# Optimization experiments

Measured on AMD Instinct MI355X. Metric: run time of the kernel, lower is better.

Reference implementation:

```python
import jax, jax.numpy as jnp
import numpy as np

LAMB_MAX = 2.0


def cheb_conv_k2(x, edge_index, w0, w1, b):
    """PyG ChebConv with K=2, sym normalization, given lambda_max.
    out = x @ w0 + (L_hat x) @ w1 + b, where
    L_hat = (2/lmax) * (I - D^{-1/2} A D^{-1/2}) - I.
    """
    n = x.shape[0]
    src, dst = edge_index[0], edge_index[1]
    ew = jnp.ones(src.shape, x.dtype)
    deg = jax.ops.segment_sum(ew, src, num_segments=n)
    dinv = jnp.where(deg > 0, jax.lax.rsqrt(jnp.maximum(deg, 1e-12)), 0.0)
    s = 2.0 / LAMB_MAX
    # off-diagonal weights of scaled Laplacian: -s * d_i^{-1/2} d_j^{-1/2}
    norm = (-s) * dinv[src] * dinv[dst]  # [E]
    # gather-scale-scatter: (L_hat x)_offdiag
    agg = jax.ops.segment_sum(norm[:, None] * x[src], dst, num_segments=n)  # [N, F]
    tx1 = (s - 1.0) * x + agg  # diagonal: s*1 (L diag) + (-1) self-loop
    return x @ w0 + tx1 @ w1 + b


def setup_inputs() -> dict:
    key = jax.random.key(0)
    ks = jax.random.split(key, 8)
    N, E, F, H = 100000, 1600000, 128, 128
    x = jax.random.normal(ks[0], (N, F), dtype=jnp.float32)
    edge_index = jax.random.randint(ks[1], (2, E), 0, N, dtype=jnp.int32)
    # glorot-ish init for the two Chebyshev linear weights per layer
    sc1 = (2.0 / (F + H)) ** 0.5
    sc2 = (2.0 / (H + 1)) ** 0.5
    w1_0 = jax.random.normal(ks[2], (F, H), dtype=jnp.float32) * sc1
    w1_1 = jax.random.normal(ks[3], (F, H), dtype=jnp.float32) * sc1
    b1 = jnp.zeros((H,), jnp.float32)
    w2_0 = jax.random.normal(ks[4], (H, 1), dtype=jnp.float32) * sc2
    w2_1 = jax.random.normal(ks[5], (H, 1), dtype=jnp.float32) * sc2
    b2 = jnp.zeros((1,), jnp.float32)
    return {"x": x, "edge_index": edge_index, "w1_0": w1_0, "w1_1": w1_1,
            "b1": b1, "w2_0": w2_0, "w2_1": w2_1, "b2": b2}


def reference(x, edge_index, w1_0, w1_1, b1, w2_0, w2_1, b2):
    h = jax.nn.relu(cheb_conv_k2(x, edge_index, w1_0, w1_1, b1))
    out = jax.nn.sigmoid(cheb_conv_k2(h, edge_index, w2_0, w2_1, b2))
    return out  # [N, 1]
```

## Files before the change

### kernel.cpp

```cpp
#include <hip/hip_runtime.h>
#include <math.h>

#define F 128
#define SCAN_CHUNK 1024
#define CHUNK 32
#define NBLK 128

typedef __attribute__((ext_vector_type(8))) short bf16x8;
typedef __attribute__((ext_vector_type(4))) float f32x4;

__device__ inline unsigned short f2bf(float v) {
  unsigned u = __float_as_uint(v);
  unsigned r = (u + 0x7FFFu + ((u >> 16) & 1u)) >> 16;
  return (unsigned short)r;
}
__device__ inline float bf2f(unsigned short s) {
  return __uint_as_float(((unsigned)s) << 16);
}

__global__ __launch_bounds__(1024) void k_prep2(const int* __restrict__ src,
                                                const int* __restrict__ dst,
                                                const float* __restrict__ x,
                                                unsigned short* __restrict__ xb,
                                                int* __restrict__ cntgD,
                                                int* __restrict__ cntgS, int E,
                                                int NF4, int nb, int per) {
  extern __shared__ int smem[];
  int* cd = smem;
  int* cs = smem + nb;
  int blk = blockIdx.x;
  int tid = threadIdx.x;
  for (int b = tid; b < nb; b += 1024) {
    cd[b] = 0;
    cs[b] = 0;
  }
  __syncthreads();
  int e0 = blk * per;
  int e1 = e0 + per;
  if (e1 > E) e1 = E;
  for (int e = e0 + tid; e < e1; e += 1024) {
    atomicAdd(&cd[dst[e] >> 7], 1);
    atomicAdd(&cs[src[e] >> 7], 1);
  }
  const float4* x4 = (const float4*)x;
  ushort4* xb4 = (ushort4*)xb;
  for (int i = blk * 1024 + tid; i < NF4; i += NBLK * 1024) {
    float4 v = x4[i];
    ushort4 o;
    o.x = f2bf(v.x);
    o.y = f2bf(v.y);
    o.z = f2bf(v.z);
    o.w = f2bf(v.w);
    xb4[i] = o;
  }
  __syncthreads();
  for (int b = tid; b < nb; b += 1024) {
    cntgD[b * NBLK + blk] = cd[b];
    cntgS[b * NBLK + blk] = cs[b];
  }
}

__global__ __launch_bounds__(NBLK) void k_scanBk2(int* __restrict__ cntgD,
                                                  int* __restrict__ cntgS,
                                                  int* __restrict__ totD,
                                                  int* __restrict__ totS, int nb) {
  __shared__ int sh[NBLK];
  int b = blockIdx.x;
  int tid = threadIdx.x;
  int* cntg;
  int* tot;
  int bb;
  if (b < nb) {
    cntg = cntgD;
    tot = totD;
    bb = b;
  } else {
    cntg = cntgS;
    tot = totS;
    bb = b - nb;
  }
  int v = cntg[bb * NBLK + tid];
  int val = v;
  sh[tid] = val;
  __syncthreads();
  for (int off = 1; off < NBLK; off <<= 1) {
    int o = (tid >= off) ? sh[tid - off] : 0;
    __syncthreads();
    val += o;
    sh[tid] = val;
    __syncthreads();
  }
  cntg[bb * NBLK + tid] = val - v;
  if (tid == NBLK - 1) tot[bb] = val;
}

__global__ __launch_bounds__(1024) void k_scanTot(const int* __restrict__ totD,
                                                  const int* __restrict__ totS,
                                                  int* __restrict__ baseD,
                                                  int* __restrict__ baseS, int nb,
                                                  int E) {
  __shared__ int sh[1024];
  int tid = threadIdx.x;
  int v = (tid < nb) ? totD[tid] : 0;
  int val = v;
  sh[tid] = val;
  __syncthreads();
  for (int off = 1; off < 1024; off <<= 1) {
    int o = (tid >= off) ? sh[tid - off] : 0;
    __syncthreads();
    val += o;
    sh[tid] = val;
    __syncthreads();
  }
  if (tid < nb) baseD[tid] = val - v;
  if (tid == 0) baseD[nb] = E;
  __syncthreads();
  v = (tid < nb) ? totS[tid] : 0;
  val = v;
  sh[tid] = val;
  __syncthreads();
  for (int off = 1; off < 1024; off <<= 1) {
    int o = (tid >= off) ? sh[tid - off] : 0;
    __syncthreads();
    val += o;
    sh[tid] = val;
    __syncthreads();
  }
  if (tid < nb) baseS[tid] = val - v;
  if (tid == 0) baseS[nb] = E;
}

__global__ __launch_bounds__(1024) void k_binfill2(
    const int* __restrict__ src, const int* __restrict__ dst,
    const int* __restrict__ cntgD, const int* __restrict__ cntgS,
    const int* __restrict__ baseD, const int* __restrict__ baseS,
    unsigned* __restrict__ binnedD, unsigned char* __restrict__ binnedS, int E,
    int nb, int per) {
  extern __shared__ int smem[];
  int* bD = smem;
  int* cD = smem + nb;
  int* bS = smem + 2 * nb;
  int* cS = smem + 3 * nb;
  int blk = blockIdx.x;
  for (int b = threadIdx.x; b < nb; b += 1024) {
    bD[b] = baseD[b] + cntgD[b * NBLK + blk];
    cD[b] = 0;
    bS[b] = baseS[b] + cntgS[b * NBLK + blk];
    cS[b] = 0;
  }
  __syncthreads();
  int e0 = blk * per;
  int e1 = e0 + per;
  if (e1 > E) e1 = E;
  for (int e = e0 + threadIdx.x; e < e1; e += 1024) {
    int s = src[e];
    int d = dst[e];
    int bk = d >> 7;
    int rk = atomicAdd(&cD[bk], 1);
    binnedD[bD[bk] + rk] = ((unsigned)s << 7) | (unsigned)(d & 127);
    int bs = s >> 7;
    int rs = atomicAdd(&cS[bs], 1);
    binnedS[bS[bs] + rs] = (unsigned char)(s & 127);
  }
}

__global__ __launch_bounds__(256) void k_csr(const unsigned char* __restrict__ binnedS,
                                             const int* __restrict__ baseS,
                                             const unsigned* __restrict__ binnedD,
                                             const int* __restrict__ baseD,
                                             float* __restrict__ dinv,
                                             int* __restrict__ rp,
                                             int* __restrict__ pairs, int N, int E) {
  __shared__ int cnt[128];
  __shared__ int sc[256];
  __shared__ int cur[128];
  int b = blockIdx.x;
  int tid = threadIdx.x;
  int node0 = b << 7;
  if (tid < 128) cnt[tid] = 0;
  __syncthreads();
  int sbeg = baseS[b], send = baseS[b + 1];
  for (int j = sbeg + tid; j < send; j += 256) atomicAdd(&cnt[binnedS[j]], 1);
  __syncthreads();
  if (tid < 128) {
    int node = node0 + tid;
    if (node < N) {
      int c = cnt[tid];
      dinv[node] = c > 0 ? rsqrtf((float)c) : 0.0f;
    }
    cnt[tid] = 0;
  }
  __syncthreads();
  int wbeg = baseD[b], wend = baseD[b + 1];
  for (int j = wbeg + tid; j < wend; j += 256) atomicAdd(&cnt[binnedD[j] & 127u], 1);
  __syncthreads();
  int v = (tid < 128) ? cnt[tid] : 0;
  int val = v;
  sc[tid] = val;
  __syncthreads();
  for (int off = 1; off < 128; off <<= 1) {
    int o = (tid >= off) ? sc[tid - off] : 0;
    __syncthreads();
    val += o;
    sc[tid] = val;
    __syncthreads();
  }
  if (tid < 128) {
    int excl = wbeg + val - v;
    int node = node0 + tid;
    if (node < N) rp[node] = excl;
    cur[tid] = excl;
  }
  if (b == 0 && tid == 0) rp[N] = E;
  __syncthreads();
  for (int j = wbeg + tid; j < wend; j += 256) {
    unsigned e = binnedD[j];
    int idx = atomicAdd(&cur[e & 127u], 1);
    pairs[idx] = (int)(e >> 7);
  }
}

__global__ __launch_bounds__(256) void k_prep(const int* __restrict__ src,
                                              const int* __restrict__ dst,
                                              const float* __restrict__ x,
                                              int* __restrict__ degA,
                                              int* __restrict__ degB,
                                              unsigned short* __restrict__ xb,
                                              int E, int NF4) {
  int t0 = blockIdx.x * 256 + threadIdx.x;
  int stride = gridDim.x * 256;
  for (int i = t0; i < E; i += stride) {
    atomicAdd(&degA[src[i]], 1);
    atomicAdd(&degB[dst[i]], 1);
  }
  const float4* x4 = (const float4*)x;
  ushort4* xb4 = (ushort4*)xb;
  for (int i = t0; i < NF4; i += stride) {
    float4 v = x4[i];
    ushort4 o;
    o.x = f2bf(v.x);
    o.y = f2bf(v.y);
    o.z = f2bf(v.z);
    o.w = f2bf(v.w);
    xb4[i] = o;
  }
}

__global__ __launch_bounds__(256) void k_scanA(const int* __restrict__ deg,
                                               int* __restrict__ rp,
                                               int* __restrict__ bsum, int N) {
  __shared__ int sh[256];
  int tid = threadIdx.x;
  int base = blockIdx.x * SCAN_CHUNK + tid * 4;
  int v0 = 0, v1 = 0, v2 = 0, v3 = 0;
  if (base + 0 < N) v0 = deg[base + 0];
  if (base + 1 < N) v1 = deg[base + 1];
  if (base + 2 < N) v2 = deg[base + 2];
  if (base + 3 < N) v3 = deg[base + 3];
  int ts = v0 + v1 + v2 + v3;
  int val = ts;
  sh[tid] = val;
  __syncthreads();
  for (int off = 1; off < 256; off <<= 1) {
    int other = (tid >= off) ? sh[tid - off] : 0;
    __syncthreads();
    val += other;
    sh[tid] = val;
    __syncthreads();
  }
  int excl = val - ts;
  if (base + 0 < N) rp[base + 0] = excl;
  if (base + 1 < N) rp[base + 1] = excl + v0;
  if (base + 2 < N) rp[base + 2] = excl + v0 + v1;
  if (base + 3 < N) rp[base + 3] = excl + v0 + v1 + v2;
  if (tid == 255) bsum[blockIdx.x] = val;
}

__global__ __launch_bounds__(256) void k_scanB(int* __restrict__ bsum, int nb) {
  __shared__ int sh[256];
  int tid = threadIdx.x;
  int ts = (tid < nb) ? bsum[tid] : 0;
  int val = ts;
  sh[tid] = val;
  __syncthreads();
  for (int off = 1; off < 256; off <<= 1) {
    int other = (tid >= off) ? sh[tid - off] : 0;
    __syncthreads();
    val += other;
    sh[tid] = val;
    __syncthreads();
  }
  if (tid < nb) bsum[tid] = val - ts;
}

__global__ __launch_bounds__(256) void k_scanC(int* __restrict__ rp,
                                               const int* __restrict__ bsum,
                                               int* __restrict__ pos,
                                               const int* __restrict__ degA,
                                               float* __restrict__ dinv, int N,
                                               int E) {
  int i = blockIdx.x * 256 + threadIdx.x;
  if (i < N) {
    int v = rp[i] + bsum[i >> 10];
    rp[i] = v;
    pos[i] = v;
    int d = degA[i];
    dinv[i] = d > 0 ? rsqrtf((float)d) : 0.0f;
  }
  if (i == 0) rp[N] = E;
}

__global__ __launch_bounds__(256) void k_fill(const int* __restrict__ src,
                                              const int* __restrict__ dst,
                                              int* __restrict__ pos,
                                              int* __restrict__ pairs, int E) {
  for (int e = blockIdx.x * 256 + threadIdx.x; e < E; e += gridDim.x * 256) {
    int s = src[e];
    int d = dst[e];
    int idx = atomicAdd(&pos[d], 1);
    pairs[idx] = s;
  }
}

__global__ __launch_bounds__(256) void k_gather1c(
    const int* __restrict__ pairs, const int* __restrict__ rp,
    const unsigned short* __restrict__ xb, const float* __restrict__ dinv,
    unsigned short* __restrict__ tb, int N) {
  int node = (blockIdx.x * 256 + threadIdx.x) >> 5;
  if (node >= N) return;
  int li = threadIdx.x & 31;
  int beg = rp[node], end = rp[node + 1];
  const uint2* x2 = (const uint2*)xb;
  float a0 = 0.f, a1 = 0.f, a2 = 0.f, a3 = 0.f;
  int j = beg;
  for (; j + 3 < end; j += 4) {
    int s0 = pairs[j], s1 = pairs[j + 1], s2 = pairs[j + 2], s3 = pairs[j + 3];
    float w0 = dinv[s0], w1 = dinv[s1], w2 = dinv[s2], w3 = dinv[s3];
    uint2 v0 = x2[(size_t)s0 * 32 + li];
    uint2 v1 = x2[(size_t)s1 * 32 + li];
    uint2 v2 = x2[(size_t)s2 * 32 + li];
    uint2 v3 = x2[(size_t)s3 * 32 + li];
    a0 += w0 * bf2f((unsigned short)v0.x) + w1 * bf2f((unsigned short)v1.x) +
          w2 * bf2f((unsigned short)v2.x) + w3 * bf2f((unsigned short)v3.x);
    a1 += w0 * bf2f((unsigned short)(v0.x >> 16)) +
          w1 * bf2f((unsigned short)(v1.x >> 16)) +
          w2 * bf2f((unsigned short)(v2.x >> 16)) +
          w3 * bf2f((unsigned short)(v3.x >> 16));
    a2 += w0 * bf2f((unsigned short)v0.y) + w1 * bf2f((unsigned short)v1.y) +
          w2 * bf2f((unsigned short)v2.y) + w3 * bf2f((unsigned short)v3.y);
    a3 += w0 * bf2f((unsigned short)(v0.y >> 16)) +
          w1 * bf2f((unsigned short)(v1.y >> 16)) +
          w2 * bf2f((unsigned short)(v2.y >> 16)) +
          w3 * bf2f((unsigned short)(v3.y >> 16));
  }
  for (; j < end; ++j) {
    int s0 = pairs[j];
    float w0 = dinv[s0];
    uint2 v0 = x2[(size_t)s0 * 32 + li];
    a0 += w0 * bf2f((unsigned short)v0.x);
    a1 += w0 * bf2f((unsigned short)(v0.x >> 16));
    a2 += w0 * bf2f((unsigned short)v0.y);
    a3 += w0 * bf2f((unsigned short)(v0.y >> 16));
  }
  float nd = -dinv[node];
  uint2 o;
  o.x = ((unsigned)f2bf(nd * a1) << 16) | f2bf(nd * a0);
  o.y = ((unsigned)f2bf(nd * a3) << 16) | f2bf(nd * a2);
  ((uint2*)tb)[(size_t)node * 32 + li] = o;
}

__global__ __launch_bounds__(256) void k_layer_mfma(
    const unsigned short* __restrict__ xb, const unsigned short* __restrict__ tb,
    const float* __restrict__ dinv, const float* __restrict__ w10,
    const float* __restrict__ w11, const float* __restrict__ b1,
    const float* __restrict__ w20, const float* __restrict__ w21,
    float* __restrict__ p, float* __restrict__ r, int N) {
  __shared__ __align__(16) short Ax[8 * 16 * 40];
  __shared__ __align__(16) short At[8 * 16 * 40];
  __shared__ float p_sh[CHUNK], r_sh[CHUNK];

  const int tid = threadIdx.x;
  const int wave = tid >> 6;
  const int lane = tid & 63;
  const int quad = lane >> 4;
  const int col = lane & 15;

  bf16x8 B0[4][2], B1[4][2];
  float b1f[2], w20f[2], w21f[2];
#pragma unroll
  for (int nt = 0; nt < 2; ++nt) {
    int f = wave * 32 + nt * 16 + col;
    b1f[nt] = b1[f];
    w20f[nt] = w20[f];
    w21f[nt] = w21[f];
  }
#pragma unroll
  for (int ks = 0; ks < 4; ++ks) {
#pragma unroll
    for (int nt = 0; nt < 2; ++nt) {
      int f = wave * 32 + nt * 16 + col;
      bf16x8 h0, h1;
#pragma unroll
      for (int j = 0; j < 8; ++j) {
        h0[j] = (short)f2bf(w10[(ks * 32 + quad * 8 + j) * F + f]);
        h1[j] = (short)f2bf(w11[(ks * 32 + quad * 8 + j) * F + f]);
      }
      B0[ks][nt] = h0;
      B1[ks][nt] = h1;
    }
  }

  const int nchunks = (N + CHUNK - 1) / CHUNK;
  for (int chunk = blockIdx.x; chunk < nchunks; chunk += gridDim.x) {
    int node0 = chunk * CHUNK;
    __syncthreads();

    {
      int nloc = tid >> 3;
      int k0 = (tid & 7) * 16;
      int gn = node0 + nloc;
      int mt = nloc >> 4, m = nloc & 15, ks = k0 >> 5, koff = k0 & 31;
      int base = ((mt * 4 + ks) * 16 + m) * 40 + koff;
      const uint2* xr = (const uint2*)(xb + (size_t)gn * F + k0);
      const uint2* tr = (const uint2*)(tb + (size_t)gn * F + k0);
      bool ok = (gn < N);
#pragma unroll
      for (int q4 = 0; q4 < 4; ++q4) {
        uint2 xv = ok ? xr[q4] : make_uint2(0u, 0u);
        uint2 tv = ok ? tr[q4] : make_uint2(0u, 0u);
        *(uint2*)&Ax[base + q4 * 4] = xv;
        *(uint2*)&At[base + q4 * 4] = tv;
      }
      if (tid < CHUNK) {
        p_sh[tid] = 0.f;
        r_sh[tid] = 0.f;
      }
    }
    __syncthreads();

    f32x4 acc[2][2];
#pragma unroll
    for (int mt = 0; mt < 2; ++mt)
#pragma unroll
      for (int nt = 0; nt < 2; ++nt) acc[mt][nt] = (f32x4)0.f;

#pragma unroll
    for (int mt = 0; mt < 2; ++mt) {
#pragma unroll
      for (int ks = 0; ks < 4; ++ks) {
        int ab = ((mt * 4 + ks) * 16 + col) * 40 + quad * 8;
        bf16x8 ax = *(bf16x8*)&Ax[ab];
        bf16x8 at = *(bf16x8*)&At[ab];
#pragma unroll
        for (int nt = 0; nt < 2; ++nt) {
          f32x4 c = acc[mt][nt];
          c = __builtin_amdgcn_mfma_f32_16x16x32_bf16(ax, B0[ks][nt], c, 0, 0, 0);
          c = __builtin_amdgcn_mfma_f32_16x16x32_bf16(at, B1[ks][nt], c, 0, 0, 0);
          acc[mt][nt] = c;
        }
      }
    }

#pragma unroll
    for (int mt = 0; mt < 2; ++mt) {
      float pp[4], rr[4];
#pragma unroll
      for (int reg = 0; reg < 4; ++reg) {
        float h0 = fmaxf(acc[mt][0][reg] + b1f[0], 0.f);
        float h1 = fmaxf(acc[mt][1][reg] + b1f[1], 0.f);
        pp[reg] = h0 * w20f[0] + h1 * w20f[1];
        rr[reg] = h0 * w21f[0] + h1 * w21f[1];
      }
#pragma unroll
      for (int off = 1; off < 16; off <<= 1) {
#pragma unroll
        for (int reg = 0; reg < 4; ++reg) {
          pp[reg] += __shfl_xor(pp[reg], off);
          rr[reg] += __shfl_xor(rr[reg], off);
        }
      }
      if (col == 0) {
#pragma unroll
        for (int reg = 0; reg < 4; ++reg) {
          atomicAdd(&p_sh[mt * 16 + quad * 4 + reg], pp[reg]);
          atomicAdd(&r_sh[mt * 16 + quad * 4 + reg], rr[reg]);
        }
      }
    }
    __syncthreads();
    if (tid < CHUNK) {
      int gn = node0 + tid;
      if (gn < N) {
        p[gn] = p_sh[tid];
        r[gn] = dinv[gn] * r_sh[tid];
      }
    }
  }
}

__global__ __launch_bounds__(256) void k_gather2_final(
    const int* __restrict__ pairs, const int* __restrict__ rp,
    const float* __restrict__ r2, const float* __restrict__ p,
    const float* __restrict__ dinv, const float* __restrict__ b2,
    float* __restrict__ out, int N) {
  int i = blockIdx.x * 256 + threadIdx.x;
  if (i >= N) return;
  int beg = rp[i], end = rp[i + 1];
  float a = 0.f;
  for (int j = beg; j < end; ++j) a += r2[pairs[j]];
  float z = p[i] - dinv[i] * a + b2[0];
  out[i] = 1.0f / (1.0f + expf(-z));
}

extern "C" void kernel_launch(void* const* d_in, const int* in_sizes, int n_in,
                              void* d_out, int out_size, void* d_ws, size_t ws_size,
                              hipStream_t stream) {
  const float* x = (const float*)d_in[0];
  const int* ei = (const int*)d_in[1];
  const float* w10 = (const float*)d_in[2];
  const float* w11 = (const float*)d_in[3];
  const float* b1 = (const float*)d_in[4];
  const float* w20 = (const float*)d_in[5];
  const float* w21 = (const float*)d_in[6];
  const float* b2 = (const float*)d_in[7];
  float* out = (float*)d_out;
  int N = in_sizes[0] / F;
  int E = in_sizes[1] / 2;
  const int* src = ei;
  const int* dst = ei + E;
  int nbuckets = (N + 127) >> 7;

  size_t off = 0;
  char* base = (char*)d_ws;
  auto take = [&](size_t bytes) {
    void* ptr = base + off;
    off += (bytes + 15) & ~(size_t)15;
    return ptr;
  };
  float* dinv = (float*)take((size_t)N * 4);
  float* p = (float*)take((size_t)N * 4);
  float* r = (float*)take((size_t)N * 4);
  int* rp = (int*)take(((size_t)N + 1) * 4);
  int* degA = (int*)take((size_t)N * 4);
  int* degB = (int*)take((size_t)N * 4);
  int* pos = (int*)take((size_t)N * 4);
  int* bsum = (int*)take(256 * 4);
  int* cntgD = (int*)take((size_t)nbuckets * NBLK * 4);
  int* cntgS = (int*)take((size_t)nbuckets * NBLK * 4);
  int* totD = (int*)take(((size_t)nbuckets + 1) * 4);
  int* totS = (int*)take(((size_t)nbuckets + 1) * 4);
  int* baseD = (int*)take(((size_t)nbuckets + 1) * 4);
  int* baseS = (int*)take(((size_t)nbuckets + 1) * 4);
  int* pairs = (int*)take((size_t)E * 4);
  unsigned short* xb = (unsigned short*)take((size_t)N * F * 2);
  unsigned short* tb = (unsigned short*)take((size_t)N * F * 2);
  if (off > ws_size) return;
  unsigned* binnedD = (unsigned*)tb;
  unsigned char* binnedS = (unsigned char*)tb + (((size_t)E * 4 + 255) & ~(size_t)255);

  int NF4 = N * (F / 4);
  int per = (E + NBLK - 1) / NBLK;

  if (nbuckets <= 1024 && (size_t)E * 5 + 256 <= (size_t)N * F * 2) {
    k_prep2<<<NBLK, 1024, (size_t)nbuckets * 8, stream>>>(src, dst, x, xb, cntgD,
                                                          cntgS, E, NF4, nbuckets,
                                                          per);
    k_scanBk2<<<2 * nbuckets, NBLK, 0, stream>>>(cntgD, cntgS, totD, totS, nbuckets);
    k_scanTot<<<1, 1024, 0, stream>>>(totD, totS, baseD, baseS, nbuckets, E);
    k_binfill2<<<NBLK, 1024, (size_t)nbuckets * 16, stream>>>(
        src, dst, cntgD, cntgS, baseD, baseS, binnedD, binnedS, E, nbuckets, per);
    k_csr<<<nbuckets, 256, 0, stream>>>(binnedS, baseS, binnedD, baseD, dinv, rp,
                                        pairs, N, E);
  } else {
    int nb_scan = (N + SCAN_CHUNK - 1) / SCAN_CHUNK;
    hipMemsetAsync(degA, 0, 2 * (size_t)N * sizeof(int), stream);
    k_prep<<<2048, 256, 0, stream>>>(src, dst, x, degA, degB, xb, E, NF4);
    k_scanA<<<nb_scan, 256, 0, stream>>>(degB, rp, bsum, N);
    k_scanB<<<1, 256, 0, stream>>>(bsum, nb_scan);
    k_scanC<<<(N + 255) / 256, 256, 0, stream>>>(rp, bsum, pos, degA, dinv, N, E);
    k_fill<<<2048, 256, 0, stream>>>(src, dst, pos, pairs, E);
  }
  k_gather1c<<<(N + 7) / 8, 256, 0, stream>>>(pairs, rp, xb, dinv, tb, N);
  k_layer_mfma<<<512, 256, 0, stream>>>(xb, tb, dinv, w10, w11, b1, w20, w21, p, r,
                                        N);
  k_gather2_final<<<(N + 255) / 256, 256, 0, stream>>>(pairs, rp, r, p, dinv, b2,
                                                       out, N);
}
```

Baseline: 299.9 us.

## Split first-layer gather into four feature-slice launches with edge-parallel lanes

The first-layer neighbor aggregation kernel now processes only a 32-feature slice per launch. Within each node's group of 32 lanes, 4 edge subgroups each cover 8 lanes of features, and partial sums are combined with xor shuffles. Four launches cover all features, so each launch touches only a quarter of every bf16 row, shrinking the working set so more of it may stay in cache. The cost is four times as many reads of the CSR indices and dinv, extra launch overhead, and shuffle reductions.

After: 407.3 us. +35.8%, slower.

```diff
diff --git a/kernel.cpp b/kernel.cpp
--- a/kernel.cpp
+++ b/kernel.cpp
@@ -322,51 +322,42 @@
   }
 }
 
-__global__ __launch_bounds__(256) void k_gather1c(
+__global__ __launch_bounds__(256) void k_gather_slice(
     const int* __restrict__ pairs, const int* __restrict__ rp,
     const unsigned short* __restrict__ xb, const float* __restrict__ dinv,
-    unsigned short* __restrict__ tb, int N) {
+    unsigned short* __restrict__ tb, int N, int slice) {
   int node = (blockIdx.x * 256 + threadIdx.x) >> 5;
   if (node >= N) return;
   int li = threadIdx.x & 31;
+  int es = li >> 3;
+  int fl = li & 7;
   int beg = rp[node], end = rp[node + 1];
   const uint2* x2 = (const uint2*)xb;
+  int soff = slice * 8 + fl;
   float a0 = 0.f, a1 = 0.f, a2 = 0.f, a3 = 0.f;
-  int j = beg;
-  for (; j + 3 < end; j += 4) {
-    int s0 = pairs[j], s1 = pairs[j + 1], s2 = pairs[j + 2], s3 = pairs[j + 3];
-    float w0 = dinv[s0], w1 = dinv[s1], w2 = dinv[s2], w3 = dinv[s3];
-    uint2 v0 = x2[(size_t)s0 * 32 + li];
-    uint2 v1 = x2[(size_t)s1 * 32 + li];
-    uint2 v2 = x2[(size_t)s2 * 32 + li];
-    uint2 v3 = x2[(size_t)s3 * 32 + li];
-    a0 += w0 * bf2f((unsigned short)v0.x) + w1 * bf2f((unsigned short)v1.x) +
-          w2 * bf2f((unsigned short)v2.x) + w3 * bf2f((unsigned short)v3.x);
-    a1 += w0 * bf2f((unsigned short)(v0.x >> 16)) +
-          w1 * bf2f((unsigned short)(v1.x >> 16)) +
-          w2 * bf2f((unsigned short)(v2.x >> 16)) +
-          w3 * bf2f((unsigned short)(v3.x >> 16));
-    a2 += w0 * bf2f((unsigned short)v0.y) + w1 * bf2f((unsigned short)v1.y) +
-          w2 * bf2f((unsigned short)v2.y) + w3 * bf2f((unsigned short)v3.y);
-    a3 += w0 * bf2f((unsigned short)(v0.y >> 16)) +
-          w1 * bf2f((unsigned short)(v1.y >> 16)) +
-          w2 * bf2f((unsigned short)(v2.y >> 16)) +
-          w3 * bf2f((unsigned short)(v3.y >> 16));
-  }
-  for (; j < end; ++j) {
-    int s0 = pairs[j];
-    float w0 = dinv[s0];
-    uint2 v0 = x2[(size_t)s0 * 32 + li];
-    a0 += w0 * bf2f((unsigned short)v0.x);
-    a1 += w0 * bf2f((unsigned short)(v0.x >> 16));
-    a2 += w0 * bf2f((unsigned short)v0.y);
-    a3 += w0 * bf2f((unsigned short)(v0.y >> 16));
-  }
-  float nd = -dinv[node];
-  uint2 o;
-  o.x = ((unsigned)f2bf(nd * a1) << 16) | f2bf(nd * a0);
-  o.y = ((unsigned)f2bf(nd * a3) << 16) | f2bf(nd * a2);
-  ((uint2*)tb)[(size_t)node * 32 + li] = o;
+  for (int j = beg + es; j < end; j += 4) {
+    int s = pairs[j];
+    float w = dinv[s];
+    uint2 v = x2[(size_t)s * 32 + soff];
+    a0 += w * bf2f((unsigned short)v.x);
+    a1 += w * bf2f((unsigned short)(v.x >> 16));
+    a2 += w * bf2f((unsigned short)v.y);
+    a3 += w * bf2f((unsigned short)(v.y >> 16));
+  }
+#pragma unroll
+  for (int off = 8; off <= 16; off <<= 1) {
+    a0 += __shfl_xor(a0, off);
+    a1 += __shfl_xor(a1, off);
+    a2 += __shfl_xor(a2, off);
+    a3 += __shfl_xor(a3, off);
+  }
+  if (es == 0) {
+    float nd = -dinv[node];
+    uint2 o;
+    o.x = ((unsigned)f2bf(nd * a1) << 16) | f2bf(nd * a0);
+    o.y = ((unsigned)f2bf(nd * a3) << 16) | f2bf(nd * a2);
+    ((uint2*)tb)[(size_t)node * 32 + soff] = o;
+  }
 }
 
 __global__ __launch_bounds__(256) void k_layer_mfma(
@@ -580,7 +571,10 @@
     k_scanC<<<(N + 255) / 256, 256, 0, stream>>>(rp, bsum, pos, degA, dinv, N, E);
     k_fill<<<2048, 256, 0, stream>>>(src, dst, pos, pairs, E);
   }
-  k_gather1c<<<(N + 7) / 8, 256, 0, stream>>>(pairs, rp, xb, dinv, tb, N);
+  int gblocks = (int)(((size_t)N * 32 + 255) / 256);
+  for (int slice = 0; slice < 4; ++slice) {
+    k_gather_slice<<<gblocks, 256, 0, stream>>>(pairs, rp, xb, dinv, tb, N, slice);
+  }
   k_layer_mfma<<<512, 256, 0, stream>>>(xb, tb, dinv, w10, w11, b1, w20, w21, p, r,
                                         N);
   k_gather2_final<<<(N + 255) / 256, 256, 0, stream>>>(pairs, rp, r, p, dinv, b2,
```
